# Performance work log

Hardware: AMD Instinct MI355X
Metric: run time of the kernel (lower is better)

## Reference

```python
import jax, jax.numpy as jnp
import numpy as np

N_NODES = 100000
N_EDGES = 3200000
FEAT = 128  # 2 * hidden_dim (hidden_dim = 64)


def setup_inputs() -> dict:
    key = jax.random.key(0)
    ks = jax.random.split(key, 8)
    x = jax.random.normal(ks[0], (N_NODES, FEAT), dtype=jnp.float32)
    x0 = jax.random.normal(ks[1], (N_NODES, FEAT), dtype=jnp.float32)
    adj_vals = jax.random.uniform(ks[2], (N_EDGES,), dtype=jnp.float32)
    alpha_train = jax.random.normal(ks[3], (N_NODES,), dtype=jnp.float32)
    w = jax.random.normal(ks[4], (FEAT, FEAT), dtype=jnp.float32)
    d = jax.random.uniform(ks[5], (FEAT,), dtype=jnp.float32)
    adj_rows = jnp.sort(jax.random.randint(ks[6], (N_EDGES,), 0, N_NODES, dtype=jnp.int32))
    adj_cols = jax.random.randint(ks[7], (N_EDGES,), 0, N_NODES, dtype=jnp.int32)
    return {
        "x": x, "x0": x0, "adj_vals": adj_vals, "alpha_train": alpha_train,
        "w": w, "d": d, "adj_rows": adj_rows, "adj_cols": adj_cols,
    }


def reference(x, x0, adj_vals, alpha_train, w, d, adj_rows, adj_cols):
    # alph = sigmoid(alpha_train).unsqueeze(1)  -> [N, 1]
    alph = jax.nn.sigmoid(alpha_train)[:, None]
    # ax = spmm(adj, x): gather source features, scale by edge value, scatter-add to rows
    ax = jax.ops.segment_sum(adj_vals[:, None] * x[adj_cols],  # [E, F]
                             adj_rows, num_segments=N_NODES)    # [N, F]
    # w_eff = (w * clamp(d, 0, 1)) @ w^T  -> [F, F]
    d_c = jnp.clip(d, 0.0, 1.0)
    w_eff = (w * d_c) @ w.T
    xw = x @ w_eff  # [N, F]
    # f = alph * 0.5 * (ax - x) + xw - x + x0
    f = alph * 0.5 * (ax - x) + xw - x + x0
    return f
```

## Files before the change

### kernel.cpp

```cpp
#include <hip/hip_runtime.h>
#include <math.h>

#define FEAT 128
#define RPB 16

#if __has_builtin(__builtin_amdgcn_cvt_pk_f32_fp8) && \
    __has_builtin(__builtin_amdgcn_cvt_pk_fp8_f32)
#define DEV_HAVE_FP8 1
#else
#define DEV_HAVE_FP8 0
#endif

typedef __attribute__((ext_vector_type(2))) float f32x2;

__global__ __launch_bounds__(256) void cvt_fp8_kernel(const float* __restrict__ x,
                                                      uint4* __restrict__ xq,
                                                      int nthreads_total) {
#if DEV_HAVE_FP8
    int t = blockIdx.x * 256 + threadIdx.x;
    if (t >= nthreads_total) return;
    const float4* xp = reinterpret_cast<const float4*>(x) + (size_t)t * 4;
    float4 a = xp[0], b = xp[1], c = xp[2], d = xp[3];
    uint4 o;
    o.x = __builtin_amdgcn_cvt_pk_fp8_f32(a.x, a.y, 0u, 0);
    o.x = __builtin_amdgcn_cvt_pk_fp8_f32(a.z, a.w, o.x, 1);
    o.y = __builtin_amdgcn_cvt_pk_fp8_f32(b.x, b.y, 0u, 0);
    o.y = __builtin_amdgcn_cvt_pk_fp8_f32(b.z, b.w, o.y, 1);
    o.z = __builtin_amdgcn_cvt_pk_fp8_f32(c.x, c.y, 0u, 0);
    o.z = __builtin_amdgcn_cvt_pk_fp8_f32(c.z, c.w, o.z, 1);
    o.w = __builtin_amdgcn_cvt_pk_fp8_f32(d.x, d.y, 0u, 0);
    o.w = __builtin_amdgcn_cvt_pk_fp8_f32(d.z, d.w, o.w, 1);
    xq[t] = o;
#endif
}

__global__ __launch_bounds__(FEAT) void weff_kernel(const float* __restrict__ w,
                                                    const float* __restrict__ d,
                                                    float* __restrict__ weff) {
    __shared__ float wT[FEAT * FEAT];
    __shared__ float as[FEAT];
    const int i = blockIdx.x;
    const int k = threadIdx.x;

    for (int j = 0; j < FEAT; j += 4) {
        float4 v = *reinterpret_cast<const float4*>(&w[k * FEAT + j]);
        wT[(j + 0) * FEAT + k] = v.x;
        wT[(j + 1) * FEAT + k] = v.y;
        wT[(j + 2) * FEAT + k] = v.z;
        wT[(j + 3) * FEAT + k] = v.w;
    }
    float dk = d[k];
    dk = fminf(fmaxf(dk, 0.0f), 1.0f);
    as[k] = w[i * FEAT + k] * dk;
    __syncthreads();

    float acc = 0.0f;
#pragma unroll 8
    for (int j = 0; j < FEAT; ++j)
        acc = fmaf(as[j], wT[j * FEAT + k], acc);
    weff[i * FEAT + k] = acc;
}

__global__ void rowptr_kernel(const int* __restrict__ rows, int* __restrict__ rp,
                              int E, int N) {
    int e = blockIdx.x * blockDim.x + threadIdx.x;
    if (e >= E) return;
    int r = rows[e];
    int rprev = (e == 0) ? -1 : rows[e - 1];
    for (int rr = rprev + 1; rr <= r; ++rr) rp[rr] = e;
    if (e == E - 1) {
        for (int rr = r + 1; rr <= N; ++rr) rp[rr] = E;
    }
}

#define SEL4(arr, base) \
    (sel2 ? (sel1 ? arr[(base) + 3] : arr[(base) + 2]) \
          : (sel1 ? arr[(base) + 1] : arr[(base) + 0]))

#if DEV_HAVE_FP8
#define FMA8(vv, gg)                                                        \
    do {                                                                    \
        f32x2 p_;                                                           \
        p_ = __builtin_amdgcn_cvt_pk_f32_fp8((gg).x, 0);                    \
        acc[0] = fmaf((vv), p_.x, acc[0]);                                  \
        acc[1] = fmaf((vv), p_.y, acc[1]);                                  \
        p_ = __builtin_amdgcn_cvt_pk_f32_fp8((gg).x, 1);                    \
        acc[2] = fmaf((vv), p_.x, acc[2]);                                  \
        acc[3] = fmaf((vv), p_.y, acc[3]);                                  \
        p_ = __builtin_amdgcn_cvt_pk_f32_fp8((gg).y, 0);                    \
        acc[4] = fmaf((vv), p_.x, acc[4]);                                  \
        acc[5] = fmaf((vv), p_.y, acc[5]);                                  \
        p_ = __builtin_amdgcn_cvt_pk_f32_fp8((gg).y, 1);                    \
        acc[6] = fmaf((vv), p_.x, acc[6]);                                  \
        acc[7] = fmaf((vv), p_.y, acc[7]);                                  \
    } while (0)
#endif

template <bool FP8>
__global__ __launch_bounds__(256, 8) void fused_kernel(
    const float* __restrict__ x, const unsigned char* __restrict__ xq,
    const float* __restrict__ x0, const float* __restrict__ vals,
    const float* __restrict__ alpha, const int* __restrict__ cols,
    const int* __restrict__ rp, const float* __restrict__ weff,
    float* __restrict__ out, int N) {
    __shared__ float xs[RPB][FEAT];
    __shared__ float axs[RPB][FEAT];

    const int tid = threadIdx.x;
    const int lane = tid & 63;
    const int wid = tid >> 6;
    const int rbase = blockIdx.x * RPB;

#pragma unroll
    for (int t = 0; t < 2; ++t) {
        int idx = t * 256 + tid;
        int row = idx >> 5, off = idx & 31;
        if (rbase + row < N) {
            *reinterpret_cast<float4*>(&xs[row][off * 4]) =
                *reinterpret_cast<const float4*>(&x[(size_t)(rbase + row) * FEAT + off * 4]);
        }
    }

#if DEV_HAVE_FP8
    if (FP8) {
        const int grp = lane >> 4;
        const int fl = lane & 15;
        const bool sel1 = (grp & 1) != 0;
        const bool sel2 = (grp & 2) != 0;

        for (int i = 0; i < 4; ++i) {
            const int r = rbase + wid * 4 + i;
            if (r >= N) break;
            const int e0 = __builtin_amdgcn_readfirstlane(rp[r]);
            const int e1 = __builtin_amdgcn_readfirstlane(rp[r + 1]);
            float acc[8] = {0.f, 0.f, 0.f, 0.f, 0.f, 0.f, 0.f, 0.f};
            int e = e0;
            for (; e + 16 <= e1; e += 16) {
                int c[16];
                float v[16];
#pragma unroll
                for (int k = 0; k < 16; ++k) {
                    c[k] = cols[e + k];
                    v[k] = vals[e + k];
                }
                int colA = SEL4(c, 0), colB = SEL4(c, 4);
                int colC = SEL4(c, 8), colD = SEL4(c, 12);
                float vA = SEL4(v, 0), vB = SEL4(v, 4);
                float vC = SEL4(v, 8), vD = SEL4(v, 12);
                uint2 gA = *reinterpret_cast<const uint2*>(&xq[(size_t)colA * FEAT + fl * 8]);
                uint2 gB = *reinterpret_cast<const uint2*>(&xq[(size_t)colB * FEAT + fl * 8]);
                uint2 gC = *reinterpret_cast<const uint2*>(&xq[(size_t)colC * FEAT + fl * 8]);
                uint2 gD = *reinterpret_cast<const uint2*>(&xq[(size_t)colD * FEAT + fl * 8]);
                FMA8(vA, gA);
                FMA8(vB, gB);
                FMA8(vC, gC);
                FMA8(vD, gD);
            }
            for (; e + 8 <= e1; e += 8) {
                int c[8];
                float v[8];
#pragma unroll
                for (int k = 0; k < 8; ++k) {
                    c[k] = cols[e + k];
                    v[k] = vals[e + k];
                }
                int colA = SEL4(c, 0), colB = SEL4(c, 4);
                float vA = SEL4(v, 0), vB = SEL4(v, 4);
                uint2 gA = *reinterpret_cast<const uint2*>(&xq[(size_t)colA * FEAT + fl * 8]);
                uint2 gB = *reinterpret_cast<const uint2*>(&xq[(size_t)colB * FEAT + fl * 8]);
                FMA8(vA, gA);
                FMA8(vB, gB);
            }
            for (; e < e1; e += 4) {
                int c[4];
                float v[4];
#pragma unroll
                for (int k = 0; k < 4; ++k) {
                    int ek = (e + k < e1) ? (e + k) : e0;
                    c[k] = cols[ek];
                    v[k] = (e + k < e1) ? vals[ek] : 0.0f;
                }
                int colA = SEL4(c, 0);
                float vA = SEL4(v, 0);
                uint2 gA = *reinterpret_cast<const uint2*>(&xq[(size_t)colA * FEAT + fl * 8]);
                FMA8(vA, gA);
            }
#pragma unroll
            for (int k = 0; k < 8; ++k) {
                acc[k] += __shfl_xor(acc[k], 16);
                acc[k] += __shfl_xor(acc[k], 32);
            }
            if (grp == 0) {
                float4 o0 = make_float4(acc[0], acc[1], acc[2], acc[3]);
                float4 o1 = make_float4(acc[4], acc[5], acc[6], acc[7]);
                *reinterpret_cast<float4*>(&axs[wid * 4 + i][fl * 8 + 0]) = o0;
                *reinterpret_cast<float4*>(&axs[wid * 4 + i][fl * 8 + 4]) = o1;
            }
        }
    } else
#endif
    {
        for (int i = 0; i < 4; ++i) {
            const int r = rbase + wid * 4 + i;
            if (r >= N) break;
            const int e0 = __builtin_amdgcn_readfirstlane(rp[r]);
            const int e1 = __builtin_amdgcn_readfirstlane(rp[r + 1]);
            float ax0 = 0.f, ax1 = 0.f;
            for (int e = e0; e < e1; ++e) {
                int c = cols[e];
                float v = vals[e];
                float2 g = *reinterpret_cast<const float2*>(
                    &x[(size_t)c * FEAT + lane * 2]);
                ax0 = fmaf(v, g.x, ax0);
                ax1 = fmaf(v, g.y, ax1);
            }
            axs[wid * 4 + i][lane * 2 + 0] = ax0;
            axs[wid * 4 + i][lane * 2 + 1] = ax1;
        }
    }
    __syncthreads();

    const int f = tid & 127;
    const int g8 = (tid >> 7) * 8;
    float xw[8] = {0.f, 0.f, 0.f, 0.f, 0.f, 0.f, 0.f, 0.f};
    for (int j = 0; j < FEAT; j += 2) {
        float w0 = weff[(j + 0) * FEAT + f];
        float w1 = weff[(j + 1) * FEAT + f];
#pragma unroll
        for (int i = 0; i < 8; ++i) {
            xw[i] = fmaf(xs[g8 + i][j + 0], w0, xw[i]);
            xw[i] = fmaf(xs[g8 + i][j + 1], w1, xw[i]);
        }
    }

#pragma unroll
    for (int i = 0; i < 8; ++i) {
        int r = rbase + g8 + i;
        if (r < N) {
            float al = 1.0f / (1.0f + __expf(-alpha[r]));
            float xv = xs[g8 + i][f];
            float o = al * 0.5f * (axs[g8 + i][f] - xv) + xw[i] - xv +
                      x0[(size_t)r * FEAT + f];
            out[(size_t)r * FEAT + f] = o;
        }
    }
}

extern "C" void kernel_launch(void* const* d_in, const int* in_sizes, int n_in,
                              void* d_out, int out_size, void* d_ws, size_t ws_size,
                              hipStream_t stream) {
    const float* x     = (const float*)d_in[0];
    const float* x0    = (const float*)d_in[1];
    const float* vals  = (const float*)d_in[2];
    const float* alpha = (const float*)d_in[3];
    const float* w     = (const float*)d_in[4];
    const float* d     = (const float*)d_in[5];
    const int*   rows  = (const int*)d_in[6];
    const int*   cols  = (const int*)d_in[7];

    const int N = in_sizes[3];
    const int E = in_sizes[2];

    const size_t rp_off = 64 * 1024;
    const size_t xq_off = (rp_off + (size_t)(N + 1) * 4 + 255) & ~255ULL;
    const size_t need = xq_off + (size_t)N * FEAT;

    float*         weff = (float*)d_ws;
    int*           rp   = (int*)((char*)d_ws + rp_off);
    unsigned char* xq   = (unsigned char*)((char*)d_ws + xq_off);
    const bool use_fp8 = (ws_size >= need);

    weff_kernel<<<FEAT, FEAT, 0, stream>>>(w, d, weff);
    rowptr_kernel<<<(E + 255) / 256, 256, 0, stream>>>(rows, rp, E, N);

    const int nblocks = (N + RPB - 1) / RPB;
    if (use_fp8) {
        int nt = (N * FEAT) / 16;
        cvt_fp8_kernel<<<(nt + 255) / 256, 256, 0, stream>>>(x, (uint4*)xq, nt);
        fused_kernel<true><<<nblocks, 256, 0, stream>>>(
            x, xq, x0, vals, alpha, cols, rp, weff, (float*)d_out, N);
    } else {
        fused_kernel<false><<<nblocks, 256, 0, stream>>>(
            x, xq, x0, vals, alpha, cols, rp, weff, (float*)d_out, N);
    }
}
```

Measured before the change: 155.4 us.

## Use split-bf16 MFMA for dense x@w_eff and vectorize SpMM index loads

The dense x @ w_eff product in the fused kernel moves from scalar FMAs to MFMA bf16 instructions. Operands are split into hi/lo bf16 pairs and combined with three MFMAs to keep close to fp32 accuracy. The SpMM gather loop now aligns to 4 edges and loads cols/vals as int4/float4 per lane group, with a 32-edge unrolled main loop, replacing scalar loads and select chains. Shared arrays get padded strides and launch bounds drop to 6 waves per SIMD. The trade-off is extra split arithmetic, lower occupancy, and a small precision loss from the split-bf16 approximation.

```diff
diff --git a/kernel.cpp b/kernel.cpp
--- a/kernel.cpp
+++ b/kernel.cpp
@@ -3,6 +3,8 @@
 
 #define FEAT 128
 #define RPB 16
+#define XS_STRIDE 136
+#define AXS_STRIDE 132
 
 #if __has_builtin(__builtin_amdgcn_cvt_pk_f32_fp8) && \
     __has_builtin(__builtin_amdgcn_cvt_pk_fp8_f32)
@@ -12,6 +14,8 @@
 #endif
 
 typedef __attribute__((ext_vector_type(2))) float f32x2;
+typedef __attribute__((ext_vector_type(4))) float f32x4;
+typedef __attribute__((ext_vector_type(8))) short bf16x8;
 
 __global__ __launch_bounds__(256) void cvt_fp8_kernel(const float* __restrict__ x,
                                                       uint4* __restrict__ xq,
@@ -36,7 +40,8 @@
 
 __global__ __launch_bounds__(FEAT) void weff_kernel(const float* __restrict__ w,
                                                     const float* __restrict__ d,
-                                                    float* __restrict__ weff) {
+                                                    unsigned short* __restrict__ wT_hi,
+                                                    unsigned short* __restrict__ wT_lo) {
     __shared__ float wT[FEAT * FEAT];
     __shared__ float as[FEAT];
     const int i = blockIdx.x;
@@ -58,7 +63,11 @@
 #pragma unroll 8
     for (int j = 0; j < FEAT; ++j)
         acc = fmaf(as[j], wT[j * FEAT + k], acc);
-    weff[i * FEAT + k] = acc;
+
+    unsigned u = __float_as_uint(acc);
+    wT_hi[(size_t)k * FEAT + i] = (unsigned short)(u >> 16);
+    float rem = acc - __uint_as_float(u & 0xffff0000u);
+    wT_lo[(size_t)k * FEAT + i] = (unsigned short)(__float_as_uint(rem) >> 16);
 }
 
 __global__ void rowptr_kernel(const int* __restrict__ rows, int* __restrict__ rp,
@@ -72,10 +81,6 @@
         for (int rr = r + 1; rr <= N; ++rr) rp[rr] = E;
     }
 }
-
-#define SEL4(arr, base) \
-    (sel2 ? (sel1 ? arr[(base) + 3] : arr[(base) + 2]) \
-          : (sel1 ? arr[(base) + 1] : arr[(base) + 0]))
 
 #if DEV_HAVE_FP8
 #define FMA8(vv, gg)                                                        \
@@ -96,15 +101,21 @@
     } while (0)
 #endif
 
+#define LDROW(c) (*reinterpret_cast<const uint2*>(&xq[(size_t)(c) * FEAT + fl * 8]))
+#define XSV(rl, f)                                                              \
+    (__uint_as_float(((unsigned)xs_hi[(rl) * XS_STRIDE + (f)]) << 16) +         \
+     __uint_as_float(((unsigned)xs_lo[(rl) * XS_STRIDE + (f)]) << 16))
+
 template <bool FP8>
-__global__ __launch_bounds__(256, 8) void fused_kernel(
+__global__ __launch_bounds__(256, 6) void fused_kernel(
     const float* __restrict__ x, const unsigned char* __restrict__ xq,
     const float* __restrict__ x0, const float* __restrict__ vals,
     const float* __restrict__ alpha, const int* __restrict__ cols,
-    const int* __restrict__ rp, const float* __restrict__ weff,
-    float* __restrict__ out, int N) {
-    __shared__ float xs[RPB][FEAT];
-    __shared__ float axs[RPB][FEAT];
+    const int* __restrict__ rp, const unsigned short* __restrict__ wT_hi,
+    const unsigned short* __restrict__ wT_lo, float* __restrict__ out, int N) {
+    __shared__ float axs[RPB * AXS_STRIDE];
+    __shared__ unsigned short xs_hi[RPB * XS_STRIDE];
+    __shared__ unsigned short xs_lo[RPB * XS_STRIDE];
 
     const int tid = threadIdx.x;
     const int lane = tid & 63;
@@ -114,10 +125,24 @@
 #pragma unroll
     for (int t = 0; t < 2; ++t) {
         int idx = t * 256 + tid;
-        int row = idx >> 5, off = idx & 31;
+        int row = idx >> 5, off = (idx & 31) * 4;
         if (rbase + row < N) {
-            *reinterpret_cast<float4*>(&xs[row][off * 4]) =
-                *reinterpret_cast<const float4*>(&x[(size_t)(rbase + row) * FEAT + off * 4]);
+            float4 v = *reinterpret_cast<const float4*>(
+                &x[(size_t)(rbase + row) * FEAT + off]);
+            float vv[4] = {v.x, v.y, v.z, v.w};
+            unsigned short hh[4], ll[4];
+#pragma unroll
+            for (int q = 0; q < 4; ++q) {
+                unsigned u = __float_as_uint(vv[q]);
+                hh[q] = (unsigned short)(u >> 16);
+                float rem = vv[q] - __uint_as_float(u & 0xffff0000u);
+                ll[q] = (unsigned short)(__float_as_uint(rem) >> 16);
+            }
+            ushort4 h, l;
+            h.x = hh[0]; h.y = hh[1]; h.z = hh[2]; h.w = hh[3];
+            l.x = ll[0]; l.y = ll[1]; l.z = ll[2]; l.w = ll[3];
+            *reinterpret_cast<ushort4*>(&xs_hi[row * XS_STRIDE + off]) = h;
+            *reinterpret_cast<ushort4*>(&xs_lo[row * XS_STRIDE + off]) = l;
         }
     }
 
@@ -135,54 +160,49 @@
             const int e1 = __builtin_amdgcn_readfirstlane(rp[r + 1]);
             float acc[8] = {0.f, 0.f, 0.f, 0.f, 0.f, 0.f, 0.f, 0.f};
             int e = e0;
+            int nh = (4 - (e & 3)) & 3;
+            if (nh > e1 - e) nh = e1 - e;
+            if (nh > 0) {
+                int ee = e + (grp < nh ? grp : nh - 1);
+                int cA = cols[ee];
+                float vA = (grp < nh) ? vals[ee] : 0.f;
+                uint2 gA = LDROW(cA);
+                FMA8(vA, gA);
+                e += nh;
+            }
+            for (; e + 32 <= e1; e += 32) {
+                int4 ca = *reinterpret_cast<const int4*>(&cols[e + grp * 4]);
+                int4 cb = *reinterpret_cast<const int4*>(&cols[e + 16 + grp * 4]);
+                float4 va = *reinterpret_cast<const float4*>(&vals[e + grp * 4]);
+                float4 vb = *reinterpret_cast<const float4*>(&vals[e + 16 + grp * 4]);
+                uint2 g0 = LDROW(ca.x), g1 = LDROW(ca.y);
+                uint2 g2 = LDROW(ca.z), g3 = LDROW(ca.w);
+                uint2 g4 = LDROW(cb.x), g5 = LDROW(cb.y);
+                uint2 g6 = LDROW(cb.z), g7 = LDROW(cb.w);
+                FMA8(va.x, g0); FMA8(va.y, g1); FMA8(va.z, g2); FMA8(va.w, g3);
+                FMA8(vb.x, g4); FMA8(vb.y, g5); FMA8(vb.z, g6); FMA8(vb.w, g7);
+            }
             for (; e + 16 <= e1; e += 16) {
-                int c[16];
-                float v[16];
-#pragma unroll
-                for (int k = 0; k < 16; ++k) {
-                    c[k] = cols[e + k];
-                    v[k] = vals[e + k];
-                }
-                int colA = SEL4(c, 0), colB = SEL4(c, 4);
-                int colC = SEL4(c, 8), colD = SEL4(c, 12);
-                float vA = SEL4(v, 0), vB = SEL4(v, 4);
-                float vC = SEL4(v, 8), vD = SEL4(v, 12);
-                uint2 gA = *reinterpret_cast<const uint2*>(&xq[(size_t)colA * FEAT + fl * 8]);
-                uint2 gB = *reinterpret_cast<const uint2*>(&xq[(size_t)colB * FEAT + fl * 8]);
-                uint2 gC = *reinterpret_cast<const uint2*>(&xq[(size_t)colC * FEAT + fl * 8]);
-                uint2 gD = *reinterpret_cast<const uint2*>(&xq[(size_t)colD * FEAT + fl * 8]);
+                int4 ca = *reinterpret_cast<const int4*>(&cols[e + grp * 4]);
+                float4 va = *reinterpret_cast<const float4*>(&vals[e + grp * 4]);
+                uint2 g0 = LDROW(ca.x), g1 = LDROW(ca.y);
+                uint2 g2 = LDROW(ca.z), g3 = LDROW(ca.w);
+                FMA8(va.x, g0); FMA8(va.y, g1); FMA8(va.z, g2); FMA8(va.w, g3);
+            }
+            for (; e + 4 <= e1; e += 4) {
+                int4 c4 = *reinterpret_cast<const int4*>(&cols[e]);
+                float4 v4 = *reinterpret_cast<const float4*>(&vals[e]);
+                int cA = sel2 ? (sel1 ? c4.w : c4.z) : (sel1 ? c4.y : c4.x);
+                float vA = sel2 ? (sel1 ? v4.w : v4.z) : (sel1 ? v4.y : v4.x);
+                uint2 gA = LDROW(cA);
                 FMA8(vA, gA);
-                FMA8(vB, gB);
-                FMA8(vC, gC);
-                FMA8(vD, gD);
-            }
-            for (; e + 8 <= e1; e += 8) {
-                int c[8];
-                float v[8];
-#pragma unroll
-                for (int k = 0; k < 8; ++k) {
-                    c[k] = cols[e + k];
-                    v[k] = vals[e + k];
-                }
-                int colA = SEL4(c, 0), colB = SEL4(c, 4);
-                float vA = SEL4(v, 0), vB = SEL4(v, 4);
-                uint2 gA = *reinterpret_cast<const uint2*>(&xq[(size_t)colA * FEAT + fl * 8]);
-                uint2 gB = *reinterpret_cast<const uint2*>(&xq[(size_t)colB * FEAT + fl * 8]);
-                FMA8(vA, gA);
-                FMA8(vB, gB);
-            }
-            for (; e < e1; e += 4) {
-                int c[4];
-                float v[4];
-#pragma unroll
-                for (int k = 0; k < 4; ++k) {
-                    int ek = (e + k < e1) ? (e + k) : e0;
-                    c[k] = cols[ek];
-                    v[k] = (e + k < e1) ? vals[ek] : 0.0f;
-                }
-                int colA = SEL4(c, 0);
-                float vA = SEL4(v, 0);
-                uint2 gA = *reinterpret_cast<const uint2*>(&xq[(size_t)colA * FEAT + fl * 8]);
+            }
+            if (e < e1) {
+                int nt = e1 - e;
+                int ee = e + (grp < nt ? grp : nt - 1);
+                int cA = cols[ee];
+                float vA = (grp < nt) ? vals[ee] : 0.f;
+                uint2 gA = LDROW(cA);
                 FMA8(vA, gA);
             }
 #pragma unroll
@@ -193,8 +213,8 @@
             if (grp == 0) {
                 float4 o0 = make_float4(acc[0], acc[1], acc[2], acc[3]);
                 float4 o1 = make_float4(acc[4], acc[5], acc[6], acc[7]);
-                *reinterpret_cast<float4*>(&axs[wid * 4 + i][fl * 8 + 0]) = o0;
-                *reinterpret_cast<float4*>(&axs[wid * 4 + i][fl * 8 + 4]) = o1;
+                *reinterpret_cast<float4*>(&axs[(wid * 4 + i) * AXS_STRIDE + fl * 8 + 0]) = o0;
+                *reinterpret_cast<float4*>(&axs[(wid * 4 + i) * AXS_STRIDE + fl * 8 + 4]) = o1;
             }
         }
     } else
@@ -209,39 +229,60 @@
             for (int e = e0; e < e1; ++e) {
                 int c = cols[e];
                 float v = vals[e];
-                float2 g = *reinterpret_cast<const float2*>(
-                    &x[(size_t)c * FEAT + lane * 2]);
+                float2 g = *reinterpret_cast<const float2*>(&x[(size_t)c * FEAT + lane * 2]);
                 ax0 = fmaf(v, g.x, ax0);
                 ax1 = fmaf(v, g.y, ax1);
             }
-            axs[wid * 4 + i][lane * 2 + 0] = ax0;
-            axs[wid * 4 + i][lane * 2 + 1] = ax1;
+            axs[(wid * 4 + i) * AXS_STRIDE + lane * 2 + 0] = ax0;
+            axs[(wid * 4 + i) * AXS_STRIDE + lane * 2 + 1] = ax1;
         }
     }
     __syncthreads();
 
-    const int f = tid & 127;
-    const int g8 = (tid >> 7) * 8;
-    float xw[8] = {0.f, 0.f, 0.f, 0.f, 0.f, 0.f, 0.f, 0.f};
-    for (int j = 0; j < FEAT; j += 2) {
-        float w0 = weff[(j + 0) * FEAT + f];
-        float w1 = weff[(j + 1) * FEAT + f];
-#pragma unroll
-        for (int i = 0; i < 8; ++i) {
-            xw[i] = fmaf(xs[g8 + i][j + 0], w0, xw[i]);
-            xw[i] = fmaf(xs[g8 + i][j + 1], w1, xw[i]);
-        }
-    }
-
-#pragma unroll
-    for (int i = 0; i < 8; ++i) {
-        int r = rbase + g8 + i;
-        if (r < N) {
-            float al = 1.0f / (1.0f + __expf(-alpha[r]));
-            float xv = xs[g8 + i][f];
-            float o = al * 0.5f * (axs[g8 + i][f] - xv) + xw[i] - xv +
-                      x0[(size_t)r * FEAT + f];
-            out[(size_t)r * FEAT + f] = o;
+    {
+        const int ml = lane & 15;
+        const int kg = lane >> 4;
+        const int n0 = wid * 32;
+        f32x4 acc0 = {0.f, 0.f, 0.f, 0.f};
+        f32x4 acc1 = {0.f, 0.f, 0.f, 0.f};
+#pragma unroll
+        for (int c = 0; c < 4; ++c) {
+            const int kb = c * 32 + kg * 8;
+            bf16x8 ah = *reinterpret_cast<const bf16x8*>(&xs_hi[ml * XS_STRIDE + kb]);
+            bf16x8 al = *reinterpret_cast<const bf16x8*>(&xs_lo[ml * XS_STRIDE + kb]);
+            bf16x8 bh0 = *reinterpret_cast<const bf16x8*>(&wT_hi[(size_t)(n0 + ml) * FEAT + kb]);
+            bf16x8 bl0 = *reinterpret_cast<const bf16x8*>(&wT_lo[(size_t)(n0 + ml) * FEAT + kb]);
+            acc0 = __builtin_amdgcn_mfma_f32_16x16x32_bf16(ah, bh0, acc0, 0, 0, 0);
+            acc0 = __builtin_amdgcn_mfma_f32_16x16x32_bf16(al, bh0, acc0, 0, 0, 0);
+            acc0 = __builtin_amdgcn_mfma_f32_16x16x32_bf16(ah, bl0, acc0, 0, 0, 0);
+            bf16x8 bh1 = *reinterpret_cast<const bf16x8*>(&wT_hi[(size_t)(n0 + 16 + ml) * FEAT + kb]);
+            bf16x8 bl1 = *reinterpret_cast<const bf16x8*>(&wT_lo[(size_t)(n0 + 16 + ml) * FEAT + kb]);
+            acc1 = __builtin_amdgcn_mfma_f32_16x16x32_bf16(ah, bh1, acc1, 0, 0, 0);
+            acc1 = __builtin_amdgcn_mfma_f32_16x16x32_bf16(al, bh1, acc1, 0, 0, 0);
+            acc1 = __builtin_amdgcn_mfma_f32_16x16x32_bf16(ah, bl1, acc1, 0, 0, 0);
+        }
+
+#pragma unroll
+        for (int i = 0; i < 4; ++i) {
+            const int rl = kg * 4 + i;
+            const int r = rbase + rl;
+            if (r < N) {
+                float al5 = 0.5f / (1.0f + __expf(-alpha[r]));
+                {
+                    const int f = n0 + ml;
+                    float xv = XSV(rl, f);
+                    float o = al5 * (axs[rl * AXS_STRIDE + f] - xv) + acc0[i] - xv +
+                              x0[(size_t)r * FEAT + f];
+                    out[(size_t)r * FEAT + f] = o;
+                }
+                {
+                    const int f = n0 + 16 + ml;
+                    float xv = XSV(rl, f);
+                    float o = al5 * (axs[rl * AXS_STRIDE + f] - xv) + acc1[i] - xv +
+                              x0[(size_t)r * FEAT + f];
+                    out[(size_t)r * FEAT + f] = o;
+                }
+            }
         }
     }
 }
@@ -261,16 +302,19 @@
     const int N = in_sizes[3];
     const int E = in_sizes[2];
 
-    const size_t rp_off = 64 * 1024;
-    const size_t xq_off = (rp_off + (size_t)(N + 1) * 4 + 255) & ~255ULL;
-    const size_t need = xq_off + (size_t)N * FEAT;
-
-    float*         weff = (float*)d_ws;
-    int*           rp   = (int*)((char*)d_ws + rp_off);
-    unsigned char* xq   = (unsigned char*)((char*)d_ws + xq_off);
+    const size_t whi_off = 0;
+    const size_t wlo_off = (size_t)FEAT * FEAT * 2;
+    const size_t rp_off  = wlo_off + (size_t)FEAT * FEAT * 2;
+    const size_t xq_off  = (rp_off + (size_t)(N + 1) * 4 + 255) & ~255ULL;
+    const size_t need    = xq_off + (size_t)N * FEAT;
+
+    unsigned short* wT_hi = (unsigned short*)((char*)d_ws + whi_off);
+    unsigned short* wT_lo = (unsigned short*)((char*)d_ws + wlo_off);
+    int*            rp    = (int*)((char*)d_ws + rp_off);
+    unsigned char*  xq    = (unsigned char*)((char*)d_ws + xq_off);
     const bool use_fp8 = (ws_size >= need);
 
-    weff_kernel<<<FEAT, FEAT, 0, stream>>>(w, d, weff);
+    weff_kernel<<<FEAT, FEAT, 0, stream>>>(w, d, wT_hi, wT_lo);
     rowptr_kernel<<<(E + 255) / 256, 256, 0, stream>>>(rows, rp, E, N);
 
     const int nblocks = (N + RPB - 1) / RPB;
@@ -278,9 +322,9 @@
         int nt = (N * FEAT) / 16;
         cvt_fp8_kernel<<<(nt + 255) / 256, 256, 0, stream>>>(x, (uint4*)xq, nt);
         fused_kernel<true><<<nblocks, 256, 0, stream>>>(
-            x, xq, x0, vals, alpha, cols, rp, weff, (float*)d_out, N);
+            x, xq, x0, vals, alpha, cols, rp, wT_hi, wT_lo, (float*)d_out, N);
     } else {
         fused_kernel<false><<<nblocks, 256, 0, stream>>>(
-            x, xq, x0, vals, alpha, cols, rp, weff, (float*)d_out, N);
-    }
-}
+            x, xq, x0, vals, alpha, cols, rp, wT_hi, wT_lo, (float*)d_out, N);
+    }
+}
```

Result: no change. 153.4 us (-1.3%).
